# Performance work log

Hardware: AMD Instinct MI355X
Metric: run time of the kernel (lower is better)

The kernel has to match this reference:

```python
import jax, jax.numpy as jnp
import numpy as np

B, T, D = 2, 1024, 1024
H, DH = 16, 64          # d_head = d_model // n_heads
MAX_POS = 64


def setup_inputs() -> dict:
    key = jax.random.key(0)
    ks = jax.random.split(key, 11)
    s = 1.0 / np.sqrt(D)
    x = jax.random.normal(ks[0], (B, T, D), jnp.float32)
    Wq = jax.random.normal(ks[1], (D, D), jnp.float32) * s
    Wk = jax.random.normal(ks[2], (D, D), jnp.float32) * s
    Wv = jax.random.normal(ks[3], (D, D), jnp.float32) * s
    Wo = jax.random.normal(ks[4], (D, D), jnp.float32) * s
    bq = jnp.zeros((D,), jnp.float32)
    bk = jnp.zeros((D,), jnp.float32)
    bv = jnp.zeros((D,), jnp.float32)
    bo = jnp.zeros((D,), jnp.float32)
    pos_emb = jax.random.normal(ks[5], (H, MAX_POS, DH), jnp.float32) * 0.02
    causal_mask = jnp.triu(jnp.ones((T, T), bool), k=1)  # True = masked (j > i)
    return dict(x=x, Wq=Wq, bq=bq, Wk=Wk, bk=bk, Wv=Wv, bv=bv, Wo=Wo, bo=bo,
                pos_emb=pos_emb, causal_mask=causal_mask)


def reference(x, Wq, bq, Wk, bk, Wv, bv, Wo, bo, pos_emb, causal_mask):
    Bv, Tv, _ = x.shape
    scale = np.sqrt(DH).astype(np.float32)

    def proj(W, b):
        return (x @ W.T + b).reshape(Bv, Tv, H, DH).transpose(0, 2, 1, 3)  # (B,H,T,d)

    Q, K, V = proj(Wq, bq), proj(Wk, bk), proj(Wv, bv)

    qk = jnp.einsum('bhid,bhjd->bhij', Q, K)              # (B,H,T,T)
    gates = jax.nn.sigmoid(qk / scale)
    gates = jnp.where(causal_mask, 0.0, gates)
    cum = jnp.cumsum(gates, axis=-1)
    pos = cum[..., -1:] - cum                             # total - cumsum_left

    pos = jnp.clip(pos, 0.0, MAX_POS - 1.0)
    pos_floor = jnp.floor(pos)
    alpha = (pos - pos_floor)[..., None]                  # (B,H,T,T,1) -> broadcast
    fidx = pos_floor.astype(jnp.int32)
    cidx = jnp.clip(jnp.ceil(pos), 0, MAX_POS - 1).astype(jnp.int32)

    # q_i . PE_{i,j} via precomputed q.pos_emb table (same math, no (B,H,T,T,d) tensor)
    qpe_tab = jnp.einsum('bhid,hpd->bhip', Q, pos_emb)    # (B,H,T,MAX_POS)
    qpe_f = jnp.take_along_axis(qpe_tab, fidx, axis=-1)   # (B,H,T,T)
    qpe_c = jnp.take_along_axis(qpe_tab, cidx, axis=-1)
    q_pe = (1.0 - alpha[..., 0]) * qpe_f + alpha[..., 0] * qpe_c

    scores = (qk + q_pe) / scale
    scores = jnp.where(causal_mask, -jnp.inf, scores)
    attn = jax.nn.softmax(scores, axis=-1)

    out = jnp.einsum('bhij,bhjd->bhid', attn, V)
    out = out.transpose(0, 2, 1, 3).reshape(Bv, Tv, D)
    return out @ Wo.T + bo
```

## Files before the change

### kernel.cpp

```cpp
#include <hip/hip_runtime.h>
#include <math.h>

#define Tt 1024
#define Dd 1024
#define Hh 16
#define DHh 64
#define MAXPOS 64
#define BTt 2048

typedef short short8 __attribute__((ext_vector_type(8)));
typedef float floatx4 __attribute__((ext_vector_type(4)));

#define MFMA16 __builtin_amdgcn_mfma_f32_16x16x32_bf16

__device__ __forceinline__ unsigned short f2bf(float f) {
    unsigned u;
    __builtin_memcpy(&u, &f, 4);
    u = (u + 0x7FFFu + ((u >> 16) & 1u)) >> 16;
    return (unsigned short)u;
}
__device__ __forceinline__ float bf2fs(short s) {
    unsigned u = ((unsigned)(unsigned short)s) << 16;
    float f;
    __builtin_memcpy(&f, &u, 4);
    return f;
}
__device__ __forceinline__ float fsigm(float x) {
    return __builtin_amdgcn_rcpf(1.f + __expf(-x));
}
__device__ __forceinline__ void gl2lds16(const short* __restrict__ g, short* l) {
    __builtin_amdgcn_global_load_lds(
        (const __attribute__((address_space(1))) void*)g,
        (__attribute__((address_space(3))) void*)l,
        16, 0, 0);
}

__global__ __launch_bounds__(256) void conv_bf16(
    const float* __restrict__ x,  const float* __restrict__ W0,
    const float* __restrict__ W1, const float* __restrict__ W2,
    const float* __restrict__ W3,
    short* __restrict__ xb, short* __restrict__ w0b, short* __restrict__ w1b,
    short* __restrict__ w2b, short* __restrict__ w3b)
{
    const float* src; short* dst; int n;
    switch (blockIdx.y) {
        case 0:  src = x;  dst = xb;  n = BTt * Dd; break;
        case 1:  src = W0; dst = w0b; n = Dd * Dd;  break;
        case 2:  src = W1; dst = w1b; n = Dd * Dd;  break;
        case 3:  src = W2; dst = w2b; n = Dd * Dd;  break;
        default: src = W3; dst = w3b; n = Dd * Dd;  break;
    }
    int idx = (blockIdx.x * 256 + threadIdx.x) * 8;
    if (idx >= n) return;
    floatx4 a0 = *(const floatx4*)&src[idx];
    floatx4 a1 = *(const floatx4*)&src[idx + 4];
    short8 s;
    for (int e = 0; e < 4; ++e) {
        s[e]     = (short)f2bf(a0[e]);
        s[e + 4] = (short)f2bf(a1[e]);
    }
    *(short8*)&dst[idx] = s;
}

template <int MODE>
__device__ __forceinline__ void gemm_body(const short* __restrict__ A,
                                          const short* __restrict__ W,
                                          const float* __restrict__ bias,
                                          void* __restrict__ Cout,
                                          int N, int K)
{
    __shared__ __align__(16) short Ash[128 * 64];
    __shared__ __align__(16) short Bsh[64 * 64];
    const int t = threadIdx.x;
    const int lane = t & 63, wave = t >> 6;
    const int quad = lane >> 4, l16 = lane & 15;
    const int row0 = blockIdx.x * 128, col0 = blockIdx.y * 64;

    const int g_r = lane >> 3, g_c = (lane & 7) * 8;

    floatx4 acc[2][4];
    for (int a = 0; a < 2; ++a)
        for (int b2 = 0; b2 < 4; ++b2)
            acc[a][b2] = (floatx4){0.f, 0.f, 0.f, 0.f};

    for (int kb = 0; kb < K; kb += 64) {
        if (kb) __syncthreads();
        for (int i = 0; i < 4; ++i) {
            int rbase = (wave * 4 + i) * 8;
            gl2lds16(&A[(size_t)(row0 + rbase + g_r) * K + kb + g_c],
                     &Ash[rbase * 64]);
        }
        for (int i = 0; i < 2; ++i) {
            int rbase = (wave * 2 + i) * 8;
            gl2lds16(&W[(size_t)(col0 + rbase + g_r) * K + kb + g_c],
                     &Bsh[rbase * 64]);
        }
        __syncthreads();
        for (int ks = 0; ks < 2; ++ks) {
            short8 af[2], bfr[4];
            for (int tm = 0; tm < 2; ++tm)
                af[tm] = *(short8*)&Ash[(wave * 32 + tm * 16 + l16) * 64 + ks * 32 + quad * 8];
            for (int tn = 0; tn < 4; ++tn)
                bfr[tn] = *(short8*)&Bsh[(tn * 16 + l16) * 64 + ks * 32 + quad * 8];
            for (int tm = 0; tm < 2; ++tm)
                for (int tn = 0; tn < 4; ++tn)
                    acc[tm][tn] = MFMA16(af[tm], bfr[tn], acc[tm][tn], 0, 0, 0);
        }
    }
    for (int tm = 0; tm < 2; ++tm)
        for (int tn = 0; tn < 4; ++tn) {
            int col = col0 + tn * 16 + l16;
            float bv = bias[col];
            for (int r = 0; r < 4; ++r) {
                int row = row0 + wave * 32 + tm * 16 + quad * 4 + r;
                float v = acc[tm][tn][r] + bv;
                if (MODE == 0) ((float*)Cout)[(size_t)row * N + col] = v;
                else           ((short*)Cout)[(size_t)row * N + col] = (short)f2bf(v);
            }
        }
}

__global__ __launch_bounds__(256) void gemm_qkv(
    const short* __restrict__ xb,
    const short* __restrict__ Wqb, const short* __restrict__ Wkb,
    const short* __restrict__ Wvb,
    const float* __restrict__ bq, const float* __restrict__ bk,
    const float* __restrict__ bv,
    short* __restrict__ Qb, short* __restrict__ Kb, short* __restrict__ Vrow)
{
    if (blockIdx.z == 0)      gemm_body<1>(xb, Wqb, bq, Qb, Dd, Dd);
    else if (blockIdx.z == 1) gemm_body<1>(xb, Wkb, bk, Kb, Dd, Dd);
    else                      gemm_body<1>(xb, Wvb, bv, Vrow, Dd, Dd);
}

__global__ __launch_bounds__(256) void gemm_o(
    const short* __restrict__ A, const short* __restrict__ W,
    const float* __restrict__ bias, float* __restrict__ C)
{
    gemm_body<0>(A, W, bias, C, Dd, Dd);
}

__global__ __launch_bounds__(256) void v_transpose(
    const short* __restrict__ Vrow, short* __restrict__ Vt)
{
    __shared__ __align__(16) short L[64 * 72];
    const int t = threadIdx.x;
    const int j0 = blockIdx.x * 64, d0 = blockIdx.y * 64, b = blockIdx.z;
    for (int s = 0; s < 2; ++s) {
        int c = t * 2 + s;
        int jr = c >> 3, c8 = c & 7;
        *(short8*)&L[jr * 72 + c8 * 8] =
            *(const short8*)&Vrow[((size_t)(b * Tt + j0 + jr)) * Dd + d0 + c8 * 8];
    }
    __syncthreads();
    for (int s = 0; s < 2; ++s) {
        int c = t * 2 + s;
        int dr = c >> 3, c8 = c & 7;
        short8 v;
        for (int e = 0; e < 8; ++e) v[e] = L[(c8 * 8 + e) * 72 + dr];
        *(short8*)&Vt[((size_t)(b * Dd + d0 + dr)) * Tt + j0 + c8 * 8] = v;
    }
}

__global__ __launch_bounds__(256) void cope_attn(
    const short* __restrict__ Q, const short* __restrict__ K,
    const short* __restrict__ Vt, const float* __restrict__ PE,
    short* __restrict__ AOb)
{
    const int h = blockIdx.y, b = blockIdx.z;
    const int t = threadIdx.x, lane = t & 63, wave = t >> 6;
    const int quad = lane >> 4, l16 = lane & 15;

    __shared__ __align__(16) short SldS[32 * 264];
    __shared__ __align__(16) short KV[128 * 72];
    __shared__ short qpeB[32 * 68];
    __shared__ float lrow[32];
    float* Sld = (float*)SldS;

    const float inv_scale = 0.125f;
    const int sr = t >> 3, ss = t & 7;

    for (int phase = 0; phase < 2; ++phase) {
        const int it = (phase == 0) ? (31 - (int)blockIdx.x) : (int)blockIdx.x;
        const int i0 = it * 32;
        const int irow = i0 + sr;

        short* QtS = SldS;
        {
            int r = t >> 3, c = t & 7;
            *(short8*)&QtS[r * 72 + c * 8] =
                *(const short8*)&Q[((size_t)(b * Tt + i0 + r)) * Dd + h * DHh + c * 8];
        }
        for (int e = 0; e < 16; ++e) {
            int idx = t + 256 * e;
            int p = idx >> 6, d = idx & 63;
            KV[p * 72 + d] = (short)f2bf(PE[((size_t)h * MAXPOS + p) * DHh + d]);
        }
        __syncthreads();

        short8 qa[2][2];
        for (int rb = 0; rb < 2; ++rb)
            for (int ks = 0; ks < 2; ++ks)
                qa[rb][ks] = *(short8*)&QtS[(rb * 16 + l16) * 72 + ks * 32 + quad * 8];

        {
            int mt = wave >> 1;
            int ntA = 2 * (wave & 1), ntB = ntA + 1;
            floatx4 c0f = {0, 0, 0, 0}, c1f = {0, 0, 0, 0};
            for (int ks = 0; ks < 2; ++ks) {
                short8 b0 = *(short8*)&KV[(ntA * 16 + l16) * 72 + ks * 32 + quad * 8];
                short8 b1 = *(short8*)&KV[(ntB * 16 + l16) * 72 + ks * 32 + quad * 8];
                c0f = MFMA16(qa[mt][ks], b0, c0f, 0, 0, 0);
                c1f = MFMA16(qa[mt][ks], b1, c1f, 0, 0, 0);
            }
            for (int r = 0; r < 4; ++r) {
                qpeB[(mt * 16 + quad * 4 + r) * 68 + ntA * 16 + l16] = (short)f2bf(c0f[r]);
                qpeB[(mt * 16 + quad * 4 + r) * 68 + ntB * 16 + l16] = (short)f2bf(c1f[r]);
            }
        }

        const int JT = (i0 + 159) >> 7;
        floatx4 o0 = {0, 0, 0, 0}, o1 = {0, 0, 0, 0};
        const int pv_mt = wave >> 1;
        const int pv_ntA = 2 * (wave & 1), pv_ntB = pv_ntA + 1;
        float l_acc = 0.f;
        float rightAcc = 0.f;

        short8 kreg[4];
        for (int e = 0; e < 4; ++e) {
            int ch = t + 256 * e;
            int jr = ch >> 3, c = ch & 7;
            kreg[e] = *(const short8*)&K[((size_t)(b * Tt + (JT - 1) * 128 + jr)) * Dd + h * DHh + c * 8];
        }

        for (int jt = JT - 1; jt >= 0; --jt) {
            const int j0 = jt * 128;
            __syncthreads();
            for (int e = 0; e < 4; ++e) {
                int ch = t + 256 * e;
                int jr = ch >> 3, c = ch & 7;
                *(short8*)&KV[jr * 72 + c * 8] = kreg[e];
            }
            __syncthreads();
            {
                int ntA = 2 * wave, ntB = ntA + 1;
                floatx4 c00 = {0,0,0,0}, c01 = {0,0,0,0}, c10 = {0,0,0,0}, c11 = {0,0,0,0};
                for (int ks = 0; ks < 2; ++ks) {
                    short8 b0 = *(short8*)&KV[(ntA * 16 + l16) * 72 + ks * 32 + quad * 8];
                    short8 b1 = *(short8*)&KV[(ntB * 16 + l16) * 72 + ks * 32 + quad * 8];
                    c00 = MFMA16(qa[0][ks], b0, c00, 0, 0, 0);
                    c01 = MFMA16(qa[0][ks], b1, c01, 0, 0, 0);
                    c10 = MFMA16(qa[1][ks], b0, c10, 0, 0, 0);
                    c11 = MFMA16(qa[1][ks], b1, c11, 0, 0, 0);
                }
                for (int r = 0; r < 4; ++r) {
                    Sld[(quad * 4 + r) * 132 + ntA * 16 + l16] = c00[r];
                    Sld[(quad * 4 + r) * 132 + ntB * 16 + l16] = c01[r];
                    Sld[(16 + quad * 4 + r) * 132 + ntA * 16 + l16] = c10[r];
                    Sld[(16 + quad * 4 + r) * 132 + ntB * 16 + l16] = c11[r];
                }
            }
            __syncthreads();
            short8 vreg[4];
            for (int e = 0; e < 4; ++e) {
                int ch = t + 256 * e;
                int d = ch >> 4, c = ch & 15;
                vreg[e] = *(const short8*)&Vt[((size_t)(b * Dd + h * DHh + d)) * Tt + j0 + c * 8];
            }
            if (jt > 0) {
                for (int e = 0; e < 4; ++e) {
                    int ch = t + 256 * e;
                    int jr = ch >> 3, c = ch & 7;
                    kreg[e] = *(const short8*)&K[((size_t)(b * Tt + j0 - 128 + jr)) * Dd + h * DHh + c * 8];
                }
            }
            {
                floatx4 qv[4];
                for (int q4 = 0; q4 < 4; ++q4) {
                    short8 qraw = *(short8*)&SldS[sr * 264 + ss * 32 + q4 * 8];
                    __builtin_memcpy(&qv[q4], &qraw, 16);
                }
                float gt[16];
                float gs = 0.f;
                for (int e = 0; e < 16; ++e) {
                    int j = j0 + ss * 16 + e;
                    float qk = qv[e >> 2][e & 3];
                    float g = (j <= irow) ? fsigm(qk * inv_scale) : 0.f;
                    gt[e] = g;
                    gs += g;
                }
                float inc = gs;
                for (int d2 = 1; d2 < 8; d2 <<= 1) {
                    float n = __shfl_down(inc, d2, 64);
                    if ((lane & 7) + d2 < 8) inc += n;
                }
                float tileTot = __shfl(inc, lane & 56, 64);
                float base = rightAcc + (inc - gs);
                float run = 0.f;
                short8 p0, p1;
                for (int e = 15; e >= 0; --e) {
                    int j = j0 + ss * 16 + e;
                    float pos = base + run;
                    run += gt[e];
                    pos = fminf(fmaxf(pos, 0.f), 63.f);
                    float pf = floorf(pos);
                    float al = pos - pf;
                    int fi = (int)pf;
                    int ci = fi + 1; if (ci > 63) ci = 63;
                    float qp = (1.f - al) * bf2fs(qpeB[sr * 68 + fi]) + al * bf2fs(qpeB[sr * 68 + ci]);
                    float qk = qv[e >> 2][e & 3];
                    float p = (j <= irow) ? __expf((qk + qp) * inv_scale) : 0.f;
                    if (e < 8) p0[e] = (short)f2bf(p); else p1[e - 8] = (short)f2bf(p);
                    l_acc += p;
                }
                *(short8*)&SldS[sr * 264 + ss * 32]     = p0;
                *(short8*)&SldS[sr * 264 + ss * 32 + 8] = p1;
                rightAcc += tileTot;
            }
            for (int e = 0; e < 4; ++e) {
                int ch = t + 256 * e;
                int d = ch >> 4, c = ch & 15;
                *(short8*)&KV[d * 136 + c * 8] = vreg[e];
            }
            __syncthreads();
            for (int ks = 0; ks < 4; ++ks) {
                short8 a  = *(short8*)&SldS[(pv_mt * 16 + l16) * 264 + ks * 64
                                            + ((quad >> 1) << 5) + ((quad & 1) << 3)];
                short8 b0 = *(short8*)&KV[(pv_ntA * 16 + l16) * 136 + ks * 32 + quad * 8];
                short8 b1 = *(short8*)&KV[(pv_ntB * 16 + l16) * 136 + ks * 32 + quad * 8];
                o0 = MFMA16(a, b0, o0, 0, 0, 0);
                o1 = MFMA16(a, b1, o1, 0, 0, 0);
            }
        }
        float lr = l_acc;
        for (int d2 = 4; d2 >= 1; d2 >>= 1) lr += __shfl_xor(lr, d2, 64);
        if (ss == 0) lrow[sr] = lr;
        __syncthreads();
        for (int r = 0; r < 4; ++r) {
            int row = pv_mt * 16 + quad * 4 + r;
            float inv = __builtin_amdgcn_rcpf(lrow[row]);
            size_t off = ((size_t)(b * Tt + i0 + row)) * Dd + h * DHh;
            AOb[off + pv_ntA * 16 + l16] = (short)f2bf(o0[r] * inv);
            AOb[off + pv_ntB * 16 + l16] = (short)f2bf(o1[r] * inv);
        }
    }
}

extern "C" void kernel_launch(void* const* d_in, const int* in_sizes, int n_in,
                              void* d_out, int out_size, void* d_ws, size_t ws_size,
                              hipStream_t stream)
{
    const float* x  = (const float*)d_in[0];
    const float* Wq = (const float*)d_in[1];
    const float* bq = (const float*)d_in[2];
    const float* Wk = (const float*)d_in[3];
    const float* bk = (const float*)d_in[4];
    const float* Wv = (const float*)d_in[5];
    const float* bv = (const float*)d_in[6];
    const float* Wo = (const float*)d_in[7];
    const float* bo = (const float*)d_in[8];
    const float* pe = (const float*)d_in[9];

    short* xb   = (short*)d_ws;
    short* Wqb  = xb   + (size_t)BTt * Dd;
    short* Wkb  = Wqb  + (size_t)Dd * Dd;
    short* Wvb  = Wkb  + (size_t)Dd * Dd;
    short* Wob  = Wvb  + (size_t)Dd * Dd;
    short* Qb   = Wob  + (size_t)Dd * Dd;
    short* Kb   = Qb   + (size_t)BTt * Dd;
    short* Vrow = Kb   + (size_t)BTt * Dd;
    short* Vtg  = Vrow + (size_t)BTt * Dd;
    short* AOb  = Vtg  + (size_t)BTt * Dd;

    dim3 gc(BTt * Dd / 8 / 256, 5);
    conv_bf16<<<gc, 256, 0, stream>>>(x, Wq, Wk, Wv, Wo, xb, Wqb, Wkb, Wvb, Wob);

    dim3 gq(BTt / 128, Dd / 64, 3);
    gemm_qkv<<<gq, 256, 0, stream>>>(xb, Wqb, Wkb, Wvb, bq, bk, bv, Qb, Kb, Vrow);

    dim3 gv(Tt / 64, Dd / 64, 2);
    v_transpose<<<gv, 256, 0, stream>>>(Vrow, Vtg);

    dim3 ga(Tt / 32 / 2, Hh, 2);
    cope_attn<<<ga, 256, 0, stream>>>(Qb, Kb, Vtg, pe, AOb);

    dim3 go(BTt / 128, Dd / 64, 1);
    gemm_o<<<go, 256, 0, stream>>>(AOb, Wob, bo, (float*)d_out);
}
```

Baseline: 181.0 us.

## Double-buffer GEMM LDS tiles and shrink output-projection row tile

```diff
diff --git a/kernel.cpp b/kernel.cpp
--- a/kernel.cpp
+++ b/kernel.cpp
@@ -62,57 +62,66 @@
     *(short8*)&dst[idx] = s;
 }
 
-template <int MODE>
+template <int MODE, int TMW>
 __device__ __forceinline__ void gemm_body(const short* __restrict__ A,
                                           const short* __restrict__ W,
                                           const float* __restrict__ bias,
                                           void* __restrict__ Cout,
                                           int N, int K)
 {
-    __shared__ __align__(16) short Ash[128 * 64];
-    __shared__ __align__(16) short Bsh[64 * 64];
+    __shared__ __align__(16) short Ash[2][TMW * 64 * 64];
+    __shared__ __align__(16) short Bsh[2][64 * 64];
     const int t = threadIdx.x;
     const int lane = t & 63, wave = t >> 6;
     const int quad = lane >> 4, l16 = lane & 15;
-    const int row0 = blockIdx.x * 128, col0 = blockIdx.y * 64;
+    const int row0 = blockIdx.x * (TMW * 64), col0 = blockIdx.y * 64;
 
     const int g_r = lane >> 3, g_c = (lane & 7) * 8;
 
-    floatx4 acc[2][4];
-    for (int a = 0; a < 2; ++a)
+    floatx4 acc[TMW][4];
+    for (int a = 0; a < TMW; ++a)
         for (int b2 = 0; b2 < 4; ++b2)
             acc[a][b2] = (floatx4){0.f, 0.f, 0.f, 0.f};
 
-    for (int kb = 0; kb < K; kb += 64) {
-        if (kb) __syncthreads();
-        for (int i = 0; i < 4; ++i) {
-            int rbase = (wave * 4 + i) * 8;
-            gl2lds16(&A[(size_t)(row0 + rbase + g_r) * K + kb + g_c],
-                     &Ash[rbase * 64]);
-        }
-        for (int i = 0; i < 2; ++i) {
-            int rbase = (wave * 2 + i) * 8;
-            gl2lds16(&W[(size_t)(col0 + rbase + g_r) * K + kb + g_c],
-                     &Bsh[rbase * 64]);
-        }
-        __syncthreads();
+#define STAGE(buf, kb)                                                      \
+    do {                                                                    \
+        for (int i = 0; i < TMW * 2; ++i) {                                 \
+            int rbase = (wave * (TMW * 2) + i) * 8;                         \
+            gl2lds16(&A[(size_t)(row0 + rbase + g_r) * K + (kb) + g_c],     \
+                     &Ash[buf][rbase * 64]);                                \
+        }                                                                   \
+        for (int i = 0; i < 2; ++i) {                                       \
+            int rbase = (wave * 2 + i) * 8;                                 \
+            gl2lds16(&W[(size_t)(col0 + rbase + g_r) * K + (kb) + g_c],     \
+                     &Bsh[buf][rbase * 64]);                                \
+        }                                                                   \
+    } while (0)
+
+    const int NT = K / 64;
+    STAGE(0, 0);
+    __syncthreads();
+    for (int ts = 0; ts < NT; ++ts) {
+        const int cur = ts & 1;
+        if (ts + 1 < NT) STAGE(cur ^ 1, (ts + 1) * 64);
         for (int ks = 0; ks < 2; ++ks) {
-            short8 af[2], bfr[4];
-            for (int tm = 0; tm < 2; ++tm)
-                af[tm] = *(short8*)&Ash[(wave * 32 + tm * 16 + l16) * 64 + ks * 32 + quad * 8];
+            short8 af[TMW], bfr[4];
+            for (int tm = 0; tm < TMW; ++tm)
+                af[tm] = *(short8*)&Ash[cur][(wave * (TMW * 16) + tm * 16 + l16) * 64 + ks * 32 + quad * 8];
             for (int tn = 0; tn < 4; ++tn)
-                bfr[tn] = *(short8*)&Bsh[(tn * 16 + l16) * 64 + ks * 32 + quad * 8];
-            for (int tm = 0; tm < 2; ++tm)
+                bfr[tn] = *(short8*)&Bsh[cur][(tn * 16 + l16) * 64 + ks * 32 + quad * 8];
+            for (int tm = 0; tm < TMW; ++tm)
                 for (int tn = 0; tn < 4; ++tn)
                     acc[tm][tn] = MFMA16(af[tm], bfr[tn], acc[tm][tn], 0, 0, 0);
         }
-    }
-    for (int tm = 0; tm < 2; ++tm)
+        if (ts + 1 < NT) __syncthreads();
+    }
+#undef STAGE
+    for (int tm = 0; tm < TMW; ++tm)
         for (int tn = 0; tn < 4; ++tn) {
             int col = col0 + tn * 16 + l16;
             float bv = bias[col];
             for (int r = 0; r < 4; ++r) {
-                int row = row0 + wave * 32 + tm * 16 + quad * 4 + r;
+                int row = row0 + wave * (TMW * 16) + tm * 16 + quad * 4 + r;
                 float v = acc[tm][tn][r] + bv;
                 if (MODE == 0) ((float*)Cout)[(size_t)row * N + col] = v;
                 else           ((short*)Cout)[(size_t)row * N + col] = (short)f2bf(v);
@@ -128,16 +137,16 @@
     const float* __restrict__ bv,
     short* __restrict__ Qb, short* __restrict__ Kb, short* __restrict__ Vrow)
 {
-    if (blockIdx.z == 0)      gemm_body<1>(xb, Wqb, bq, Qb, Dd, Dd);
-    else if (blockIdx.z == 1) gemm_body<1>(xb, Wkb, bk, Kb, Dd, Dd);
-    else                      gemm_body<1>(xb, Wvb, bv, Vrow, Dd, Dd);
+    if (blockIdx.z == 0)      gemm_body<1, 2>(xb, Wqb, bq, Qb, Dd, Dd);
+    else if (blockIdx.z == 1) gemm_body<1, 2>(xb, Wkb, bk, Kb, Dd, Dd);
+    else                      gemm_body<1, 2>(xb, Wvb, bv, Vrow, Dd, Dd);
 }
 
 __global__ __launch_bounds__(256) void gemm_o(
     const short* __restrict__ A, const short* __restrict__ W,
     const float* __restrict__ bias, float* __restrict__ C)
 {
-    gemm_body<0>(A, W, bias, C, Dd, Dd);
+    gemm_body<0, 1>(A, W, bias, C, Dd, Dd);
 }
 
 __global__ __launch_bounds__(256) void v_transpose(
@@ -384,6 +393,6 @@
     dim3 ga(Tt / 32 / 2, Hh, 2);
     cope_attn<<<ga, 256, 0, stream>>>(Qb, Kb, Vtg, pe, AOb);
 
-    dim3 go(BTt / 128, Dd / 64, 1);
+    dim3 go(BTt / 64, Dd / 64, 1);
     gemm_o<<<go, 256, 0, stream>>>(AOb, Wob, bo, (float*)d_out);
 }
```

Measured after the change: 178.7 us. Within noise of the previous version (-1.3%).
